# Optimization experiments

Measured on AMD Instinct MI355X. Metric: run time of the kernel, lower is better.

The kernel has to match this reference:

```python
import jax, jax.numpy as jnp
import numpy as np

B, S, H = 4, 2048, 2048
NH, NKV, HD = 16, 8, 128
Q_SIZE, KV_SIZE = NH * HD, NKV * HD
EPS = 1e-6
BASE = 10000.0
SCALE = HD ** -0.5


def _rmsnorm(x, w):
    # per-head RMSNorm over last dim (head_dim), with learnable weight
    var = jnp.mean(x * x, axis=-1, keepdims=True)
    return x * jax.lax.rsqrt(var + EPS) * w


def _rope(x, positions):
    # neox-style rotary embedding, rotary_dim == head_dim. x: [B,S,h,HD]
    half = HD // 2
    inv_freq = 1.0 / (BASE ** (jnp.arange(half, dtype=jnp.float32) / half))
    ang = positions.astype(jnp.float32)[..., None] * inv_freq  # [B,S,half]
    cos = jnp.cos(ang)[:, :, None, :]
    sin = jnp.sin(ang)[:, :, None, :]
    x1, x2 = x[..., :half], x[..., half:]
    return jnp.concatenate([x1 * cos - x2 * sin, x2 * cos + x1 * sin], axis=-1)


def setup_inputs() -> dict:
    key = jax.random.key(0)
    k0, k1, k2 = jax.random.split(key, 3)
    return {
        "positions": jnp.tile(jnp.arange(S, dtype=jnp.int32), (B, 1)),
        "hidden_states": jax.random.normal(k0, (B, S, H), jnp.float32),
        "w_qkv": jax.random.normal(k1, (H, Q_SIZE + 2 * KV_SIZE), jnp.float32) * (H ** -0.5),
        "q_norm_w": jnp.ones((HD,), jnp.float32),
        "k_norm_w": jnp.ones((HD,), jnp.float32),
        "w_o": jax.random.normal(k2, (NH * HD, H), jnp.float32) * ((NH * HD) ** -0.5),
    }


def reference(positions, hidden_states, w_qkv, q_norm_w, k_norm_w, w_o):
    # QKV projection (bias=False)
    qkv = jnp.einsum("bsh,ho->bso", hidden_states, w_qkv)
    q, k, v = jnp.split(qkv, [Q_SIZE, Q_SIZE + KV_SIZE], axis=-1)
    q = q.reshape(B, S, NH, HD)
    k = k.reshape(B, S, NKV, HD)
    v = v.reshape(B, S, NKV, HD)
    # qk-norm (RMSNorm per head vector)
    q = _rmsnorm(q, q_norm_w)
    k = _rmsnorm(k, k_norm_w)
    # rotary embeddings
    q = _rope(q, positions)
    k = _rope(k, positions)
    # GQA: repeat kv heads to match query heads
    rep = NH // NKV
    k = jnp.repeat(k, rep, axis=2)  # [B,S,NH,HD]
    v = jnp.repeat(v, rep, axis=2)
    # bidirectional (ENCODER_ONLY) attention, no mask
    scores = jnp.einsum("bqhd,bkhd->bhqk", q, k) * SCALE
    probs = jax.nn.softmax(scores, axis=-1)
    ctx = jnp.einsum("bhqk,bkhd->bqhd", probs, v).reshape(B, S, NH * HD)
    # output projection (bias=False)
    return jnp.einsum("bso,oh->bsh", ctx, w_o)
```

## Files before the change

kernel.cpp:

```cpp
#include <hip/hip_runtime.h>

#define S_LEN 2048
#define QKV_N 4096
#define SCALE_Q_LOG2E 0.12751744461f

typedef __attribute__((ext_vector_type(8))) short short8;
typedef __attribute__((ext_vector_type(4))) float f32x4;
typedef __attribute__((ext_vector_type(16))) float f32x16;
typedef __attribute__((ext_vector_type(4))) float floatv4;
typedef __attribute__((ext_vector_type(4))) unsigned short ushortv4;
typedef __attribute__((ext_vector_type(2))) unsigned int uint2v;

__device__ __forceinline__ float bf2f(unsigned short u) {
  union { unsigned u; float f; } x; x.u = ((unsigned)u) << 16; return x.f;
}
__device__ __forceinline__ unsigned short f2bf(float f) {
  union { float f; unsigned u; } x; x.f = f;
  unsigned r = x.u + 0x7fffu + ((x.u >> 16) & 1u);
  return (unsigned short)(r >> 16);
}

typedef const unsigned int __attribute__((address_space(1)))* gas1_t;
typedef unsigned int __attribute__((address_space(3)))* las3_t;
#define GLL16(g, l) __builtin_amdgcn_global_load_lds((gas1_t)(const void*)(g), (las3_t)(void*)(l), 16, 0, 0)

#define EXP2F(x) __builtin_amdgcn_exp2f(x)

__global__ __launch_bounds__(256) void k_cvt(const float* __restrict__ in,
                                             unsigned short* __restrict__ out, int n4) {
  int i = blockIdx.x * 256 + threadIdx.x;
  if (i >= n4) return;
  floatv4 v = ((const floatv4*)in)[i];
  ushortv4 o;
  o[0] = f2bf(v[0]); o[1] = f2bf(v[1]); o[2] = f2bf(v[2]); o[3] = f2bf(v[3]);
  ((ushortv4*)out)[i] = o;
}

__global__ __launch_bounds__(256) void k_transpose_cvt(const float* __restrict__ in,
                                                       unsigned short* __restrict__ out,
                                                       int R, int C) {
  __shared__ float t[64][65];
  int bx = blockIdx.x;
  int by = blockIdx.y;
#pragma unroll
  for (int i = 0; i < 16; ++i) {
    int idx = threadIdx.x + i * 256;
    int r = idx >> 6, c = idx & 63;
    t[r][c] = in[(size_t)(by * 64 + r) * C + bx * 64 + c];
  }
  __syncthreads();
#pragma unroll
  for (int i = 0; i < 16; ++i) {
    int idx = threadIdx.x + i * 256;
    int r = idx >> 6, c = idx & 63;
    out[(size_t)(bx * 64 + r) * R + by * 64 + c] = f2bf(t[c][r]);
  }
}

template <int OUT_BF16>
__global__ __launch_bounds__(512, 2) void k_gemm256(const unsigned short* __restrict__ A,
                                                    const unsigned short* __restrict__ BT,
                                                    void* __restrict__ Cout,
                                                    int M, int N, int K) {
  const int tid = threadIdx.x;
  const int lane = tid & 63;
  const int wid = tid >> 6;
  const int wr = wid >> 2;
  const int wc = wid & 3;
  const int lr = lane & 15, lg = lane >> 4;

  const int gx = gridDim.x;
  const int nwg = gx * gridDim.y;
  const int lid = blockIdx.y * gx + blockIdx.x;
  const int qc = nwg >> 3;
  const int swz = (lid & 7) * qc + (lid >> 3);
  const int row0 = (swz / gx) * 256, col0 = (swz % gx) * 256;

  __shared__ __align__(16) unsigned short As[2][256 * 64];
  __shared__ __align__(16) unsigned short Bs[2][256 * 64];

  f32x4 acc[8][4];
#pragma unroll
  for (int m = 0; m < 8; ++m)
#pragma unroll
    for (int n = 0; n < 4; ++n) acc[m][n] = (f32x4){0.f, 0.f, 0.f, 0.f};

  const int r1 = tid >> 3, c1 = tid & 7;
  const int r2 = (tid + 512) >> 3, c2 = (tid + 512) & 7;
  const size_t so1 = (size_t)r1 * K + (size_t)((c1 ^ (r1 & 7)) * 8);
  const size_t so2 = (size_t)r2 * K + (size_t)((c2 ^ (r2 & 7)) * 8);
  const unsigned ld1 = (unsigned)tid * 16, ld2 = (unsigned)(tid + 512) * 16;

  const unsigned short* Abase = A + (size_t)row0 * K;
  const unsigned short* Bbase = BT + (size_t)col0 * K;

  auto stage = [&](int ph, int kt, int buf) {
    const size_t hb = (size_t)(ph >> 1) * 128 * K + (size_t)kt * 64;
    const unsigned short* src;
    unsigned short* dst;
    if (ph & 1) { src = Bbase + hb; dst = &Bs[buf][(ph >> 1) * 128 * 64]; }
    else        { src = Abase + hb; dst = &As[buf][(ph >> 1) * 128 * 64]; }
    GLL16(src + so1, (char*)dst + ld1);
    GLL16(src + so2, (char*)dst + ld2);
  };

#pragma unroll
  for (int ph = 0; ph < 4; ++ph) stage(ph, 0, 0);
  asm volatile("s_waitcnt vmcnt(0)" ::: "memory");
  __builtin_amdgcn_s_barrier();

  const int NT = K >> 6;
  for (int t = 0; t < NT; ++t) {
    const int cur = t & 1;
    const char* Ab = (const char*)&As[cur][0];
    const char* Bb = (const char*)&Bs[cur][0];
    short8 bf[4];
#pragma unroll
    for (int p = 0; p < 4; ++p) {
      const int ks = p >> 1, half = p & 1;
      short8 af[4];
#pragma unroll
      for (int m = 0; m < 4; ++m) {
        int rA = wr * 128 + (half * 4 + m) * 16 + lr;
        af[m] = *(const short8*)(Ab +
                ((rA * 128 + (ks * 4 + lg) * 16) ^ ((rA & 7) << 4)));
      }
      if (half == 0) {
#pragma unroll
        for (int n = 0; n < 4; ++n) {
          int rB = wc * 64 + n * 16 + lr;
          bf[n] = *(const short8*)(Bb +
                  ((rB * 128 + (ks * 4 + lg) * 16) ^ ((rB & 7) << 4)));
        }
      }
      if (t + 1 < NT) stage(p, t + 1, cur ^ 1);
      __builtin_amdgcn_sched_barrier(0);
      __builtin_amdgcn_s_setprio(1);
#pragma unroll
      for (int m = 0; m < 4; ++m)
#pragma unroll
        for (int n = 0; n < 4; ++n)
          acc[half * 4 + m][n] = __builtin_amdgcn_mfma_f32_16x16x32_bf16(
              af[m], bf[n], acc[half * 4 + m][n], 0, 0, 0);
      __builtin_amdgcn_s_setprio(0);
      if (p == 3) asm volatile("s_waitcnt vmcnt(0)" ::: "memory");
      __builtin_amdgcn_s_barrier();
    }
  }

  if (OUT_BF16) {
    unsigned short* C = (unsigned short*)Cout;
#pragma unroll
    for (int m = 0; m < 8; ++m)
#pragma unroll
      for (int n = 0; n < 4; ++n)
#pragma unroll
        for (int r = 0; r < 4; ++r)
          C[(size_t)(row0 + wr * 128 + m * 16 + 4 * lg + r) * N + col0 + wc * 64 + n * 16 + lr] =
              f2bf(acc[m][n][r]);
  } else {
    float* C = (float*)Cout;
#pragma unroll
    for (int m = 0; m < 8; ++m)
#pragma unroll
      for (int n = 0; n < 4; ++n)
#pragma unroll
        for (int r = 0; r < 4; ++r)
          C[(size_t)(row0 + wr * 128 + m * 16 + 4 * lg + r) * N + col0 + wc * 64 + n * 16 + lr] =
              acc[m][n][r];
  }
}

__global__ __launch_bounds__(256) void k_normrope(unsigned short* __restrict__ qkv,
                                                  const int* __restrict__ pos,
                                                  const float* __restrict__ qw,
                                                  const float* __restrict__ kw) {
  int lane = threadIdx.x & 63;
  int wv = (blockIdx.x << 2) + (threadIdx.x >> 6);
  int bs = wv / 24, hr = wv - bs * 24;
  bool isq = hr < 16;
  int col0 = isq ? hr * 128 : 2048 + (hr - 16) * 128;
  unsigned short* row = qkv + (size_t)bs * QKV_N + col0;
  float x1 = bf2f(row[lane]), x2 = bf2f(row[lane + 64]);
  float ss = x1 * x1 + x2 * x2;
#pragma unroll
  for (int m = 1; m < 64; m <<= 1) ss += __shfl_xor(ss, m, 64);
  float rn = rsqrtf(ss * (1.0f / 128.0f) + 1e-6f);
  const float* w = isq ? qw : kw;
  x1 *= rn * w[lane];
  x2 *= rn * w[lane + 64];
  float p = (float)pos[bs];
  float freq = exp2f(-(float)lane * 0.20762050593045951f);
  float ang = p * freq;
  float sn = __sinf(ang), cs = __cosf(ang);
  float o1 = x1 * cs - x2 * sn;
  float o2 = x2 * cs + x1 * sn;
  float sc = isq ? SCALE_Q_LOG2E : 1.0f;
  row[lane] = f2bf(o1 * sc);
  row[lane + 64] = f2bf(o2 * sc);
}

__global__ __launch_bounds__(512, 2) void k_attn(const unsigned short* __restrict__ qkv,
                                                 unsigned short* __restrict__ ctx) {
  const int tid = threadIdx.x;
  const int lane = tid & 63;
  const int wid = tid >> 6;
  const int hi = lane >> 5;
  const int l15 = lane & 15;
  const int q31 = lane & 31;
  const int lid0 = blockIdx.y * 8 + blockIdx.x;
  const int xcd = lid0 & 7, idx = lid0 >> 3;
  const int bh = xcd * 8 + (idx & 7);
  const int qb = idx >> 3;
  const int b = bh >> 4, h = bh & 15, kvh = h >> 1;

  __shared__ __align__(16) unsigned short Ks[2][64 * 128];
  __shared__ __align__(16) unsigned short Vs[2][64 * 128];

  const size_t baseRow = (size_t)b * S_LEN;
  const int qrow = qb * 256 + wid * 32 + q31;

  const unsigned short* Qg = qkv + (baseRow + qrow) * QKV_N + h * 128;
  short8 qf[8];
#pragma unroll
  for (int c = 0; c < 8; ++c)
    qf[c] = *(const short8*)(Qg + c * 16 + hi * 8);

  const unsigned short* Kg = qkv + baseRow * QKV_N + 2048 + kvh * 128;
  const unsigned short* Vg = Kg + 1024;

  size_t ksrc[2], vsrc[2];
  unsigned sdst[2];
#pragma unroll
  for (int i = 0; i < 2; ++i) {
    int s = tid + i * 512;
    int krow = s >> 4, kc = s & 15;
    ksrc[i] = (size_t)krow * QKV_N + (size_t)((kc ^ (krow & 7)) * 8);
    int st = s >> 3, in8 = s & 7;
    int vkey = (st >> 3) * 4 + (in8 >> 1);
    int vj = ((st & 7) << 1) | (in8 & 1);
    vsrc[i] = (size_t)vkey * QKV_N + (size_t)(vj * 8);
    sdst[i] = (unsigned)s * 16;
  }

#define STAGE(T, BUF)                                                    \
  {                                                                      \
    size_t toff = (size_t)(T) * 64 * QKV_N;                              \
    GLL16(Kg + toff + ksrc[0], (char*)Ks[BUF] + sdst[0]);                \
    GLL16(Kg + toff + ksrc[1], (char*)Ks[BUF] + sdst[1]);                \
    GLL16(Vg + toff + vsrc[0], (char*)Vs[BUF] + sdst[0]);                \
    GLL16(Vg + toff + vsrc[1], (char*)Vs[BUF] + sdst[1]);                \
  }

  f32x16 acc[4];
#pragma unroll
  for (int d = 0; d < 4; ++d)
#pragma unroll
    for (int r = 0; r < 16; ++r) acc[d][r] = 0.f;
  float m_run = -1e30f, l_run = 0.f;

  const unsigned vbase = (unsigned)(uintptr_t)&Vs[0][0];
  const int sw = (q31 & 7) << 4;

  auto tr_issue = [&](uint2v* vr, int ksg, unsigned vb) {
#pragma unroll
    for (int db = 0; db < 4; ++db)
#pragma unroll
      for (int rd = 0; rd < 2; ++rd) {
        int st = (ksg * 4 + hi * 2 + rd) * 8 + db * 2 + ((lane >> 4) & 1);
        unsigned a = vb + (unsigned)(st * 128 + l15 * 8);
        asm volatile("ds_read_b64_tr_b16 %0, %1" : "=v"(vr[db * 2 + rd]) : "v"(a));
      }
  };

  STAGE(0, 0);

  for (int t = 0; t < 32; ++t) {
    const int cur = t & 1;
    __builtin_amdgcn_s_barrier();
    __builtin_amdgcn_sched_barrier(0);
    if (t < 31) {
      STAGE(t + 1, cur ^ 1);
      asm volatile("s_waitcnt vmcnt(4)" ::: "memory");
    } else {
      asm volatile("s_waitcnt vmcnt(0)" ::: "memory");
    }
    __builtin_amdgcn_s_barrier();
    __builtin_amdgcn_sched_barrier(0);

    const char* Kb = (const char*)Ks[cur];
    f32x16 p0, p1;
#pragma unroll
    for (int r = 0; r < 16; ++r) { p0[r] = 0.f; p1[r] = 0.f; }
#pragma unroll
    for (int c = 0; c < 8; ++c) {
      int cb = c * 32 + hi * 16;
      short8 k0 = *(const short8*)(Kb + q31 * 256 + (cb ^ sw));
      short8 k1 = *(const short8*)(Kb + (32 + q31) * 256 + (cb ^ sw));
      p0 = __builtin_amdgcn_mfma_f32_32x32x16_bf16(k0, qf[c], p0, 0, 0, 0);
      p1 = __builtin_amdgcn_mfma_f32_32x32x16_bf16(k1, qf[c], p1, 0, 0, 0);
    }

    float mt = p0[0];
#pragma unroll
    for (int r = 1; r < 16; ++r) mt = fmaxf(mt, p0[r]);
#pragma unroll
    for (int r = 0; r < 16; ++r) mt = fmaxf(mt, p1[r]);
    mt = fmaxf(mt, __shfl_xor(mt, 32, 64));
    if (!__all(mt - m_run <= 8.0f)) {
      float mnew = fmaxf(m_run, mt);
      float corr = EXP2F(m_run - mnew);
      l_run *= corr;
#pragma unroll
      for (int d = 0; d < 4; ++d)
#pragma unroll
        for (int r = 0; r < 16; ++r) acc[d][r] *= corr;
      m_run = mnew;
    }
    float s_loc = 0.f;
#pragma unroll
    for (int r = 0; r < 16; ++r) { p0[r] = EXP2F(p0[r] - m_run); s_loc += p0[r]; }
#pragma unroll
    for (int r = 0; r < 16; ++r) { p1[r] = EXP2F(p1[r] - m_run); s_loc += p1[r]; }
    l_run += s_loc + __shfl_xor(s_loc, 32, 64);

    const unsigned vb = vbase + (unsigned)cur * 16384u;
    const float* pp0 = (const float*)&p0;
    const float* pp1 = (const float*)&p1;
    uint2v vrA[8], vrB[8];
    tr_issue(vrA, 0, vb);
#pragma unroll
    for (int ks = 0; ks < 4; ++ks) {
      const float* pr = ((ks & 2) ? pp1 : pp0) + (ks & 1) * 8;
      unsigned t0, t1, u0, u1;
      asm("v_cvt_pk_bf16_f32 %0, %1, %2" : "=v"(t0) : "v"(pr[0]), "v"(pr[1]));
      asm("v_cvt_pk_bf16_f32 %0, %1, %2" : "=v"(t1) : "v"(pr[2]), "v"(pr[3]));
      asm("v_cvt_pk_bf16_f32 %0, %1, %2" : "=v"(u0) : "v"(pr[4]), "v"(pr[5]));
      asm("v_cvt_pk_bf16_f32 %0, %1, %2" : "=v"(u1) : "v"(pr[6]), "v"(pr[7]));
      asm("v_permlane32_swap_b32 %0, %1" : "+v"(t0), "+v"(u0));
      asm("v_permlane32_swap_b32 %0, %1" : "+v"(t1), "+v"(u1));
      union { unsigned u[4]; short8 s; } pa;
      pa.u[0] = t0; pa.u[1] = t1; pa.u[2] = u0; pa.u[3] = u1;

      if (ks == 0) tr_issue(vrB, 1, vb);
      else if (ks == 1) tr_issue(vrA, 2, vb);
      else if (ks == 2) tr_issue(vrB, 3, vb);

      if (ks < 3) asm volatile("s_waitcnt lgkmcnt(8)" ::: "memory");
      else        asm volatile("s_waitcnt lgkmcnt(0)" ::: "memory");
      __builtin_amdgcn_sched_barrier(0);
#pragma unroll
      for (int db = 0; db < 4; ++db) {
        union { uint2v v[2]; short8 s; } vf;
        if (ks & 1) { vf.v[0] = vrB[db * 2]; vf.v[1] = vrB[db * 2 + 1]; }
        else        { vf.v[0] = vrA[db * 2]; vf.v[1] = vrA[db * 2 + 1]; }
        acc[db] = __builtin_amdgcn_mfma_f32_32x32x16_bf16(vf.s, pa.s, acc[db], 0, 0, 0);
      }
    }
  }

  float inv = 1.0f / l_run;
  unsigned short* Co = ctx + (baseRow + qrow) * 2048 + h * 128;
#pragma unroll
  for (int db = 0; db < 4; ++db)
#pragma unroll
    for (int g = 0; g < 4; ++g) {
      ushortv4 v;
#pragma unroll
      for (int j = 0; j < 4; ++j) v[j] = f2bf(acc[db][4 * g + j] * inv);
      *(ushortv4*)(Co + db * 32 + g * 8 + hi * 4) = v;
    }
#undef STAGE
}

extern "C" void kernel_launch(void* const* d_in, const int* in_sizes, int n_in,
                              void* d_out, int out_size, void* d_ws, size_t ws_size,
                              hipStream_t stream) {
  const int* positions = (const int*)d_in[0];
  const float* hidden = (const float*)d_in[1];
  const float* w_qkv = (const float*)d_in[2];
  const float* q_norm_w = (const float*)d_in[3];
  const float* k_norm_w = (const float*)d_in[4];
  const float* w_o = (const float*)d_in[5];
  float* out = (float*)d_out;

  char* ws = (char*)d_ws;
  unsigned short* hA    = (unsigned short*)(ws);
  unsigned short* wqkvT = (unsigned short*)(ws + 33554432);
  unsigned short* woT   = (unsigned short*)(ws + 50331648);
  unsigned short* qkv   = (unsigned short*)(ws + 58720256);
  unsigned short* ctx   = hA;

  k_cvt<<<16384, 256, 0, stream>>>(hidden, hA, (8192 * 2048) / 4);
  k_transpose_cvt<<<dim3(64, 32), 256, 0, stream>>>(w_qkv, wqkvT, 2048, 4096);
  k_transpose_cvt<<<dim3(32, 32), 256, 0, stream>>>(w_o, woT, 2048, 2048);
  k_gemm256<1><<<dim3(16, 32), 512, 0, stream>>>(hA, wqkvT, qkv, 8192, 4096, 2048);
  k_normrope<<<49152, 256, 0, stream>>>(qkv, positions, q_norm_w, k_norm_w);
  k_attn<<<dim3(8, 64), 512, 0, stream>>>(qkv, ctx);
  k_gemm256<0><<<dim3(8, 32), 512, 0, stream>>>(ctx, woT, out, 8192, 2048, 2048);
}
```

Measured before the change: 413.1 us.

## Restructure GEMM LDS pipeline into four-stage ring with K-step 32

Replaces the double-buffered 64-wide K tiles with a four-slot ring of 32-wide K tiles for A and B, prefetching three stages ahead and using counted vmcnt waits. Each iteration now has one barrier, and the new XOR swizzle matches the 64-byte row stride. The aim is to hide global-to-LDS load latency better and cut the number of barriers per K-chunk. The trade-off is a smaller MFMA batch per barrier and more in-flight loads per thread.

```diff
diff --git a/kernel.cpp b/kernel.cpp
--- a/kernel.cpp
+++ b/kernel.cpp
@@ -76,8 +76,7 @@
   const int swz = (lid & 7) * qc + (lid >> 3);
   const int row0 = (swz / gx) * 256, col0 = (swz % gx) * 256;
 
-  __shared__ __align__(16) unsigned short As[2][256 * 64];
-  __shared__ __align__(16) unsigned short Bs[2][256 * 64];
+  __shared__ __align__(16) unsigned short U[4][2][256 * 32];
 
   f32x4 acc[8][4];
 #pragma unroll
@@ -85,67 +84,56 @@
 #pragma unroll
     for (int n = 0; n < 4; ++n) acc[m][n] = (f32x4){0.f, 0.f, 0.f, 0.f};
 
-  const int r1 = tid >> 3, c1 = tid & 7;
-  const int r2 = (tid + 512) >> 3, c2 = (tid + 512) & 7;
-  const size_t so1 = (size_t)r1 * K + (size_t)((c1 ^ (r1 & 7)) * 8);
-  const size_t so2 = (size_t)r2 * K + (size_t)((c2 ^ (r2 & 7)) * 8);
+  const int ra1 = tid >> 2, ja1 = tid & 3;
+  const int ra2 = (tid + 512) >> 2, ja2 = (tid + 512) & 3;
+  const size_t so1 = (size_t)ra1 * K + (size_t)((ja1 ^ (ra1 & 3)) * 8);
+  const size_t so2 = (size_t)ra2 * K + (size_t)((ja2 ^ (ra2 & 3)) * 8);
   const unsigned ld1 = (unsigned)tid * 16, ld2 = (unsigned)(tid + 512) * 16;
 
   const unsigned short* Abase = A + (size_t)row0 * K;
   const unsigned short* Bbase = BT + (size_t)col0 * K;
 
-  auto stage = [&](int ph, int kt, int buf) {
-    const size_t hb = (size_t)(ph >> 1) * 128 * K + (size_t)kt * 64;
-    const unsigned short* src;
-    unsigned short* dst;
-    if (ph & 1) { src = Bbase + hb; dst = &Bs[buf][(ph >> 1) * 128 * 64]; }
-    else        { src = Abase + hb; dst = &As[buf][(ph >> 1) * 128 * 64]; }
-    GLL16(src + so1, (char*)dst + ld1);
-    GLL16(src + so2, (char*)dst + ld2);
+  auto stage = [&](int u) {
+    const int s = u & 3;
+    const size_t kof = (size_t)u * 32;
+    GLL16(Abase + kof + so1, (char*)&U[s][0][0] + ld1);
+    GLL16(Abase + kof + so2, (char*)&U[s][0][0] + ld2);
+    GLL16(Bbase + kof + so1, (char*)&U[s][1][0] + ld1);
+    GLL16(Bbase + kof + so2, (char*)&U[s][1][0] + ld2);
   };
 
-#pragma unroll
-  for (int ph = 0; ph < 4; ++ph) stage(ph, 0, 0);
-  asm volatile("s_waitcnt vmcnt(0)" ::: "memory");
-  __builtin_amdgcn_s_barrier();
-
-  const int NT = K >> 6;
-  for (int t = 0; t < NT; ++t) {
-    const int cur = t & 1;
-    const char* Ab = (const char*)&As[cur][0];
-    const char* Bb = (const char*)&Bs[cur][0];
-    short8 bf[4];
-#pragma unroll
-    for (int p = 0; p < 4; ++p) {
-      const int ks = p >> 1, half = p & 1;
-      short8 af[4];
-#pragma unroll
-      for (int m = 0; m < 4; ++m) {
-        int rA = wr * 128 + (half * 4 + m) * 16 + lr;
-        af[m] = *(const short8*)(Ab +
-                ((rA * 128 + (ks * 4 + lg) * 16) ^ ((rA & 7) << 4)));
-      }
-      if (half == 0) {
-#pragma unroll
-        for (int n = 0; n < 4; ++n) {
-          int rB = wc * 64 + n * 16 + lr;
-          bf[n] = *(const short8*)(Bb +
-                  ((rB * 128 + (ks * 4 + lg) * 16) ^ ((rB & 7) << 4)));
-        }
-      }
-      if (t + 1 < NT) stage(p, t + 1, cur ^ 1);
-      __builtin_amdgcn_sched_barrier(0);
-      __builtin_amdgcn_s_setprio(1);
-#pragma unroll
-      for (int m = 0; m < 4; ++m)
-#pragma unroll
-        for (int n = 0; n < 4; ++n)
-          acc[half * 4 + m][n] = __builtin_amdgcn_mfma_f32_16x16x32_bf16(
-              af[m], bf[n], acc[half * 4 + m][n], 0, 0, 0);
-      __builtin_amdgcn_s_setprio(0);
-      if (p == 3) asm volatile("s_waitcnt vmcnt(0)" ::: "memory");
-      __builtin_amdgcn_s_barrier();
-    }
+  stage(0); stage(1); stage(2);
+
+  const int NT2 = K >> 5;
+  for (int i = 0; i < NT2; ++i) {
+    if (i + 2 < NT2)      asm volatile("s_waitcnt vmcnt(8)" ::: "memory");
+    else if (i + 1 < NT2) asm volatile("s_waitcnt vmcnt(4)" ::: "memory");
+    else                  asm volatile("s_waitcnt vmcnt(0)" ::: "memory");
+    __builtin_amdgcn_s_barrier();
+    __builtin_amdgcn_sched_barrier(0);
+    if (i + 3 < NT2) stage(i + 3);
+
+    const char* Au = (const char*)&U[i & 3][0][0];
+    const char* Bu = (const char*)&U[i & 3][1][0];
+    short8 af[8], bf[4];
+#pragma unroll
+    for (int m = 0; m < 8; ++m) {
+      int rA = wr * 128 + m * 16 + lr;
+      af[m] = *(const short8*)(Au + rA * 64 + ((lg ^ (rA & 3)) << 4));
+    }
+#pragma unroll
+    for (int n = 0; n < 4; ++n) {
+      int rB = wc * 64 + n * 16 + lr;
+      bf[n] = *(const short8*)(Bu + rB * 64 + ((lg ^ (rB & 3)) << 4));
+    }
+    __builtin_amdgcn_s_setprio(1);
+#pragma unroll
+    for (int m = 0; m < 8; ++m)
+#pragma unroll
+      for (int n = 0; n < 4; ++n)
+        acc[m][n] = __builtin_amdgcn_mfma_f32_16x16x32_bf16(
+            af[m], bf[n], acc[m][n], 0, 0, 0);
+    __builtin_amdgcn_s_setprio(0);
   }
 
   if (OUT_BF16) {
```

Result: no change. 416.8 us (+0.9%).
